# Optimization experiments

Measured on AMD Instinct MI355X. Metric: run time of the kernel, lower is better.

The kernel has to match this reference:

```python
import jax, jax.numpy as jnp
import numpy as np
from itertools import combinations

A = 4          # anchor_points
K = 16         # neighbor_num
INTRA = A * (A - 1) // 2   # 6
CH = INTRA * 2 + A * A     # 28 = generator channels
B, N, S = 1, 8192, 4096
CIN, COUT = 64, 128


def cdist(x):
    # pairwise euclidean distances [B,N,N], zero-safe sqrt (zero grad at d=0)
    sq = jnp.sum(x * x, -1)
    d2 = sq[:, :, None] + sq[:, None, :] - 2.0 * jnp.einsum('bnc,bmc->bnm', x, x)
    d2 = jnp.maximum(d2, 0.0)
    m = d2 > 0
    return jnp.where(m, jnp.sqrt(jnp.where(m, d2, 1.0)), 0.0)


def index_points(points, idx):
    # points [B,N,...], idx [B,*] -> [B,*,...]
    return jax.vmap(lambda p, i: p[i])(points, idx)


def index_points_dists(dists, i1, i2):
    # dists [B,N,N]; result[b,...] = dists[b, i1[b,...], i2[b,...]]
    i1, i2 = jnp.broadcast_arrays(i1, i2)
    return jax.vmap(lambda d, a, b: d[a, b])(dists, i1, i2)


def generator(xyz):
    # RotationInvariantDistFea.forward(xyz, concat_raw_relative_fea=True)
    D = cdist(xyz)
    neg_nd, ni = jax.lax.top_k(-D, K)   # K >= A; smallest-K, sorted ascending
    nd = -neg_nd
    ai = ni[:, :, :A]
    # intra-anchor dists: dists to anchors 1..A-1 plus pairwise dists among them
    subs = [index_points_dists(D, ai[:, :, pi], ai[:, :, pj])[:, :, None]
            for pi, pj in combinations(range(1, A), 2)]
    intra = jnp.concatenate([nd[:, :, 1:A]] + subs, axis=2)  # [B,P,6]
    # inter-anchor dists: center anchors x neighbor anchors -> [B,P,K,A*A]
    nai = index_points(ai, ni)                                # [B,P,K,A]
    inter = index_points_dists(D, ai[:, :, None, :, None],
                               nai[:, :, :, None, :]).reshape(D.shape[0], D.shape[1], K, A * A)
    center = jnp.broadcast_to(intra[:, :, None, :], (intra.shape[0], intra.shape[1], K, INTRA))
    rf = jnp.concatenate([center, index_points(intra, ni), inter], axis=3)  # [B,P,K,28]
    return rf, ni, D


def mlp(x, W, b, g, be, act):
    # Linear + BatchNorm1d (training mode: stats over batch*points) + optional leaky_relu(0.2)
    y = x @ W + b
    mu = jnp.mean(y, (0, 1))
    var = jnp.var(y, (0, 1))
    y = (y - mu) * jax.lax.rsqrt(var + 1e-5) * g + be
    return jax.nn.leaky_relu(y, 0.2) if act else y


def forward(xyz, feature, sample_indexes, Ww, bw, gw, betaw, Wb, bb, gb, betab, Wo, bo, go, betao):
    rf_before, ni_before, D_before = generator(xyz)
    intra_before = rf_before[:, :, 0, :INTRA]
    xyz_s = index_points(xyz, sample_indexes)
    feat = index_points(feature, sample_indexes)
    intra_before = index_points(intra_before, sample_indexes)
    rf_after, ni_after, _ = generator(xyz_s)
    intra_after = rf_after[:, :, 0, :INTRA]
    a_before = index_points(ni_before[:, :, :A], sample_indexes)                  # [B,S,A]
    a_after = jax.vmap(lambda s, a: s[a])(sample_indexes, ni_after[:, :, :A])     # map to global idx
    inter = index_points_dists(D_before, a_before[:, :, :, None],
                               a_after[:, :, None, :]).reshape(B, S, A * A)
    adf = jnp.concatenate([intra_before, intra_after, inter], axis=2)             # [B,S,28]
    w = mlp(adf, Ww, bw, gw, betaw, False)
    bia = mlp(adf, Wb, bb, gb, betab, False)
    feat = jax.nn.leaky_relu(feat * w + bia, 0.2)
    feat = jnp.concatenate([feat, adf], axis=2)                                   # [B,S,92]
    feat = mlp(feat, Wo, bo, go, betao, True)                                     # [B,S,128]
    return xyz_s, feat, rf_after, ni_after


def setup_inputs():
    key = jax.random.key(0)
    ks = jax.random.split(key, 8)
    xyz = jax.random.normal(ks[0], (B, N, 3), jnp.float32)
    feature = jax.random.normal(ks[1], (B, N, CIN), jnp.float32)
    sample_indexes = jnp.stack([jax.random.permutation(jax.random.fold_in(ks[2], i), N)[:S]
                                for i in range(B)]).astype(jnp.int32)

    def lin(k, cin, cout):
        k1, k2 = jax.random.split(k)
        W = jax.random.normal(k1, (cin, cout), jnp.float32) / np.float32(np.sqrt(cin))
        b = jax.random.normal(k2, (cout,), jnp.float32) * 0.01
        return W, b, jnp.ones((cout,), jnp.float32), jnp.zeros((cout,), jnp.float32)

    Ww, bw, gw, betaw = lin(ks[5], CH, CIN)
    Wb, bb, gb, betab = lin(ks[6], CH, CIN)
    Wo, bo, go, betao = lin(ks[7], CH + CIN, COUT)
    return dict(xyz=xyz, feature=feature, sample_indexes=sample_indexes,
                Ww=Ww, bw=bw, gw=gw, betaw=betaw,
                Wb=Wb, bb=bb, gb=gb, betab=betab,
                Wo=Wo, bo=bo, go=go, betao=betao)


def reference(xyz, feature, sample_indexes, Ww, bw, gw, betaw, Wb, bb, gb, betab, Wo, bo, go, betao):
    return forward(xyz, feature, sample_indexes, Ww, bw, gw, betaw, Wb, bb, gb, betab, Wo, bo, go, betao)
```

## Files before the change

### kernel.cpp

```cpp
#include <hip/hip_runtime.h>
#include <hip/hip_bf16.h>
#include <math.h>

#define N_PTS 8192
#define S_PTS 4096
typedef unsigned long long u64;
typedef unsigned u32;

__device__ __forceinline__ float d2_f32_gram(const float4 a, const float4 b) {
    float dot = __fadd_rn(__fadd_rn(__fmul_rn(a.x, b.x), __fmul_rn(a.y, b.y)),
                          __fmul_rn(a.z, b.z));
    float d2 = __fsub_rn(__fadd_rn(a.w, b.w), __fmul_rn(2.0f, dot));
    return fmaxf(d2, 0.0f);
}

__device__ __forceinline__ float pair_dist_f(const float4 a, const float4 b) {
    float d2 = d2_f32_gram(a, b);
    return d2 > 0.0f ? __fsqrt_rn(d2) : 0.0f;
}

__global__ __launch_bounds__(256) void stage_kernel(
        const float* __restrict__ xyz, const int* __restrict__ sidx,
        float4* __restrict__ cb, float4* __restrict__ ca,
        float* __restrict__ out_xyz_s) {
    int i = blockIdx.x * blockDim.x + threadIdx.x;
    if (i < N_PTS) {
        float x = xyz[i * 3 + 0], y = xyz[i * 3 + 1], z = xyz[i * 3 + 2];
        float sq = __fadd_rn(__fadd_rn(__fmul_rn(x, x), __fmul_rn(y, y)),
                             __fmul_rn(z, z));
        cb[i] = make_float4(x, y, z, sq);
    }
    if (i < S_PTS) {
        int si = sidx[i];
        float x = xyz[si * 3 + 0], y = xyz[si * 3 + 1], z = xyz[si * 3 + 2];
        float sq = __fadd_rn(__fadd_rn(__fmul_rn(x, x), __fmul_rn(y, y)),
                             __fmul_rn(z, z));
        ca[i] = make_float4(x, y, z, sq);
        out_xyz_s[i * 3 + 0] = x;
        out_xyz_s[i * 3 + 1] = y;
        out_xyz_s[i * 3 + 2] = z;
    }
}


template <int KOUT, int ITERS>
__device__ u64 knn_full_ladder(const float4 q, const float4* __restrict__ cand,
                               int lane) {
    u32 Lk[KOUT], Li[KOUT];
#pragma unroll
    for (int j = 0; j < KOUT; ++j) { Lk[j] = 0xFFFFFFFFu; Li[j] = 0xFFFFFFFFu; }
    int c = lane;
    for (int tt = 0; tt < ITERS; ++tt, c += 64) {
        float d2 = d2_f32_gram(q, cand[c]);
        float Df = d2 > 0.0f ? __fsqrt_rn(d2) : 0.0f;
        u32 kb = __float_as_uint(Df);
        if (kb < Lk[KOUT - 1]) {
#pragma unroll
            for (int j = KOUT - 1; j >= 1; --j) {
                bool up = kb < Lk[j - 1], ins = kb < Lk[j];
                Lk[j] = up ? Lk[j - 1] : (ins ? kb : Lk[j]);
                Li[j] = up ? Li[j - 1] : (ins ? (u32)c : Li[j]);
            }
            bool i0 = kb < Lk[0];
            Lk[0] = i0 ? kb : Lk[0];
            Li[0] = i0 ? (u32)c : Li[0];
        }
    }
    u64 Lu[KOUT];
#pragma unroll
    for (int j = 0; j < KOUT; ++j) Lu[j] = ((u64)Lk[j] << 32) | (u64)Li[j];
    u64 res = ~0ull;
#pragma unroll
    for (int r = 0; r < KOUT; ++r) {
        u64 m = Lu[0];
#pragma unroll
        for (int off = 32; off >= 1; off >>= 1) {
            u64 o = __shfl_xor(m, off, 64);
            m = (o < m) ? o : m;
        }
        if (lane == r) res = m;
        if (Lu[0] == m) {
#pragma unroll
            for (int j = 0; j < KOUT - 1; ++j) Lu[j] = Lu[j + 1];
            Lu[KOUT - 1] = ~0ull;
        }
    }
    return res;
}

template <int K, int NC>
__device__ u64 final_select(const float4 qq, const float4* __restrict__ cand,
                            const u64* bufq, u32 cnt, int lane) {
    if (cnt <= 64u) {
        u64 v = (lane < (int)cnt) ? bufq[lane] : ~0ull;
#pragma unroll
        for (int k = 2; k <= 64; k <<= 1) {
#pragma unroll
            for (int j2 = k >> 1; j2 >= 1; j2 >>= 1) {
                u64 o = __shfl_xor(v, j2, 64);
                bool keepMin = (((lane & j2) == 0) == ((lane & k) == 0));
                bool less = o < v;
                v = keepMin ? (less ? o : v) : (less ? v : o);
            }
        }
        return v;
    } else if (cnt <= 256u) {
        u64 L0 = ~0ull, L1 = ~0ull, L2 = ~0ull, L3 = ~0ull;
        for (u32 mm = lane; mm < cnt; mm += 64) {
            u64 kk = bufq[mm];
            if (kk < L3) {
                if (kk < L1) {
                    L3 = L2; L2 = L1;
                    if (kk < L0) { L1 = L0; L0 = kk; } else L1 = kk;
                } else {
                    if (kk < L2) { L3 = L2; L2 = kk; } else L3 = kk;
                }
            }
        }
        u64 res = ~0ull;
#pragma unroll
        for (int r = 0; r < K; ++r) {
            u64 mr = L0;
#pragma unroll
            for (int off = 32; off >= 1; off >>= 1) {
                u64 o = __shfl_xor(mr, off, 64);
                mr = (o < mr) ? o : mr;
            }
            if (lane == r) res = mr;
            if (L0 == mr) { L0 = L1; L1 = L2; L2 = L3; L3 = ~0ull; }
        }
        return res;
    }
    return knn_full_ladder<K, NC / 64>(qq, cand, lane);
}

template <int J, int K, int NC, int Q>
__device__ __forceinline__ u64 knn_selectq(
        const float4* qs, const float4* __restrict__ cand, int t,
        u32* mins, u64* buf, u32* shm) {
    int lane = t & 63, wid = t >> 6;
    u32 d2b[Q][J];
    u32 m[Q];
#pragma unroll
    for (int qi = 0; qi < Q; ++qi) m[qi] = 0xFFFFFFFFu;
#pragma unroll
    for (int j = 0; j < J; ++j) {
        float4 c = cand[t + 256 * j];
#pragma unroll
        for (int qi = 0; qi < Q; ++qi) {
            u32 b = __float_as_uint(d2_f32_gram(qs[qi], c));
            d2b[qi][j] = b;
            m[qi] = b < m[qi] ? b : m[qi];
        }
    }
#pragma unroll
    for (int qi = 0; qi < Q; ++qi) mins[qi * 256 + t] = m[qi];
    __syncthreads();
    if (wid < Q) {
        const u32* mq = mins + wid * 256;
        u32 v = mq[lane];
        u32 v2 = mq[lane + 64];  v = v2 < v ? v2 : v;
        v2 = mq[lane + 128];     v = v2 < v ? v2 : v;
        v2 = mq[lane + 192];     v = v2 < v ? v2 : v;
#pragma unroll
        for (int k = 2; k <= 64; k <<= 1) {
#pragma unroll
            for (int j2 = k >> 1; j2 >= 1; j2 >>= 1) {
                u32 o = __shfl_xor(v, j2, 64);
                bool keepMin = (((lane & j2) == 0) == ((lane & k) == 0));
                bool less = o < v;
                v = keepMin ? (less ? o : v) : (less ? v : o);
            }
        }
        if (lane == K - 1) shm[wid] = v;
    }
    __syncthreads();
    u32 tau[Q], c[Q], x[Q];
#pragma unroll
    for (int qi = 0; qi < Q; ++qi) {
        tau[qi] = shm[qi];
        u32 cc = 0;
#pragma unroll
        for (int j = 0; j < J; ++j) cc += (d2b[qi][j] <= tau[qi]) ? 1u : 0u;
        c[qi] = cc;
        u32 xx = cc;
#pragma unroll
        for (int off = 1; off < 64; off <<= 1) {
            u32 y = __shfl_up(xx, off, 64);
            if (lane >= off) xx += y;
        }
        x[qi] = xx;
        if (lane == 63) shm[Q + qi * 4 + wid] = xx;
    }
    __syncthreads();
    u32 cnt[Q];
#pragma unroll
    for (int qi = 0; qi < Q; ++qi) {
        u32 base = x[qi] - c[qi];
        for (int w = 0; w < wid; ++w) base += shm[Q + qi * 4 + w];
        cnt[qi] = shm[Q + qi * 4 + 0] + shm[Q + qi * 4 + 1] +
                  shm[Q + qi * 4 + 2] + shm[Q + qi * 4 + 3];
        if (cnt[qi] <= 256u) {
            u32 off = base;
#pragma unroll
            for (int j = 0; j < J; ++j) {
                if (d2b[qi][j] <= tau[qi]) {
                    float d2 = __uint_as_float(d2b[qi][j]);
                    float D = d2 > 0.0f ? __fsqrt_rn(d2) : 0.0f;
                    buf[qi * 256 + off++] = ((u64)__float_as_uint(D) << 32) |
                                            (u64)(u32)(t + 256 * j);
                }
            }
        }
    }
    __syncthreads();
    u64 res = ~0ull;
#pragma unroll
    for (int qi = 0; qi < Q; ++qi)
        if (wid == qi)
            res = final_select<K, NC>(qs[qi], cand, buf + qi * 256, cnt[qi], lane);
    return res;
}

__global__ __launch_bounds__(256, 4) void knn_kernel(
        const float4* __restrict__ cb, const float4* __restrict__ ca,
        const int* __restrict__ sidx,
        u64* __restrict__ stage_b4,
        int* __restrict__ ni_i, float* __restrict__ intra_after,
        float* __restrict__ out_ni) {
    __shared__ u32 mins[4 * 256];
    __shared__ u64 buf[4 * 256];
    __shared__ u32 shm[24];
    int t = threadIdx.x, lane = t & 63, wid = t >> 6;
    int bid = blockIdx.x;
    if (bid < S_PTS / 4) {
        int s0 = bid * 4;
        float4 qs[4];
#pragma unroll
        for (int qi = 0; qi < 4; ++qi) qs[qi] = ca[s0 + qi];
        u64 res = knn_selectq<16, 16, 4096, 4>(qs, ca, t, mins, buf, shm);
        if (wid < 4) {
            int s = s0 + wid;
            int idx = (int)(res & 0xffffffffull);
            if (lane < 16) {
                ni_i[s * 16 + lane] = idx;
                out_ni[s * 16 + lane] = (float)idx;
            }
            if (lane >= 1 && lane < 4)
                intra_after[s * 6 + (lane - 1)] =
                    __uint_as_float((u32)(res >> 32));
            int i1 = __shfl(idx, 1, 64);
            int i2 = __shfl(idx, 2, 64);
            int i3 = __shfl(idx, 3, 64);
            if (lane < 3) {
                int pa = (lane == 2) ? i2 : i1;
                int pb = (lane == 0) ? i2 : i3;
                intra_after[s * 6 + 3 + lane] = pair_dist_f(ca[pa], ca[pb]);
            }
        }
    } else {
        int idx2 = bid - S_PTS / 4;
        int qg = idx2 >> 1;
        int h = idx2 & 1;
        int s0 = qg * 4;
        float4 qs[4];
#pragma unroll
        for (int qi = 0; qi < 4; ++qi) qs[qi] = cb[sidx[s0 + qi]];
        u64 res = knn_selectq<16, 4, 4096, 4>(qs, cb + h * 4096, t, mins, buf, shm);
        if (wid < 4 && lane < 4) {
            int s = s0 + wid;
            stage_b4[s * 8 + h * 4 + lane] = res + (u64)(h * 4096);
        }
    }
}

__device__ __forceinline__ void cswap_u64(u64& x, u64& y) {
    u64 lo = x < y ? x : y;
    u64 hi = x < y ? y : x;
    x = lo; y = hi;
}

__global__ __launch_bounds__(256) void merge_before_kernel(
        const u64* __restrict__ stage_b4, const float4* __restrict__ cb,
        int* __restrict__ a_before, float* __restrict__ intra_before) {
    int s = blockIdx.x * 256 + threadIdx.x;
    const u64* p = stage_b4 + s * 8;
    u64 a0 = p[0], a1 = p[1], a2 = p[2], a3 = p[3];
    u64 b0 = p[4], b1 = p[5], b2 = p[6], b3 = p[7];
    u64 c0 = a0 < b3 ? a0 : b3;
    u64 c1 = a1 < b2 ? a1 : b2;
    u64 c2 = a2 < b1 ? a2 : b1;
    u64 c3 = a3 < b0 ? a3 : b0;
    cswap_u64(c0, c1); cswap_u64(c2, c3);
    cswap_u64(c0, c2); cswap_u64(c1, c3);
    cswap_u64(c1, c2);
    int i0 = (int)(c0 & 0xffffffffull);
    int i1 = (int)(c1 & 0xffffffffull);
    int i2 = (int)(c2 & 0xffffffffull);
    int i3 = (int)(c3 & 0xffffffffull);
    a_before[s * 4 + 0] = i0;
    a_before[s * 4 + 1] = i1;
    a_before[s * 4 + 2] = i2;
    a_before[s * 4 + 3] = i3;
    intra_before[s * 6 + 0] = __uint_as_float((u32)(c1 >> 32));
    intra_before[s * 6 + 1] = __uint_as_float((u32)(c2 >> 32));
    intra_before[s * 6 + 2] = __uint_as_float((u32)(c3 >> 32));
    float4 p1 = cb[i1], p2 = cb[i2], p3 = cb[i3];
    intra_before[s * 6 + 3] = pair_dist_f(p1, p2);
    intra_before[s * 6 + 4] = pair_dist_f(p1, p3);
    intra_before[s * 6 + 5] = pair_dist_f(p2, p3);
}

__global__ __launch_bounds__(256) void assemble_kernel(
        const float4* __restrict__ ca, const float4* __restrict__ cb,
        const int* __restrict__ ni_i, const float* __restrict__ intra_after,
        const int* __restrict__ a_before, const float* __restrict__ intra_before,
        const int* __restrict__ sidx,
        float* __restrict__ out_rf, float* __restrict__ adf) {
    __shared__ int s_ni[4][16];
    __shared__ float s_rf[4][16 * 28];
    __shared__ float s_ia[4][8];
    int t = threadIdx.x, wid = t >> 6, lane = t & 63;
    int s = blockIdx.x * 4 + wid;
    if (lane < 16) s_ni[wid][lane] = ni_i[s * 16 + lane];
    if (lane < 6) s_ia[wid][lane] = intra_after[s * 6 + lane];
    __syncthreads();

    int k = lane >> 2, qq = lane & 3;
    int nai_q = ni_i[s_ni[wid][k] * 16 + qq];
    float4 pq = ca[nai_q];
#pragma unroll
    for (int p = 0; p < 4; ++p) {
        float4 pp = ca[s_ni[wid][p]];
        s_rf[wid][k * 28 + 12 + p * 4 + qq] = pair_dist_f(pp, pq);
    }
    for (int idx = lane; idx < 16 * 12; idx += 64) {
        int kk = idx / 12, c = idx % 12;
        float v = (c < 6) ? s_ia[wid][c] : intra_after[s_ni[wid][kk] * 6 + (c - 6)];
        s_rf[wid][kk * 28 + c] = v;
    }
    if (lane < 16) {
        int p = lane >> 2, q2 = lane & 3;
        int ib = a_before[s * 4 + p];
        int ia = sidx[s_ni[wid][q2]];
        adf[s * 28 + 12 + lane] = pair_dist_f(cb[ib], cb[ia]);
    } else if (lane >= 32 && lane < 38) {
        adf[s * 28 + (lane - 32)] = intra_before[s * 6 + (lane - 32)];
    } else if (lane >= 40 && lane < 46) {
        adf[s * 28 + 6 + (lane - 40)] = s_ia[wid][lane - 40];
    }
    __syncthreads();
    const int base = s * 16 * 28;
    for (int idx = lane; idx < 16 * 28; idx += 64) out_rf[base + idx] = s_rf[wid][idx];
}

__global__ __launch_bounds__(256) void mlp1_kernel(
        const float* __restrict__ adf,
        const float* __restrict__ Ww, const float* __restrict__ bw,
        const float* __restrict__ Wb, const float* __restrict__ bb,
        float* __restrict__ y_wb,
        float* __restrict__ part1, float* __restrict__ part2) {
    __shared__ float sW[28 * 128];
    __shared__ float sb[128];
    __shared__ float sA[32 * 28];
    __shared__ float red[32][128];
    int t = threadIdx.x;
    for (int i = t; i < 28 * 128; i += 256) {
        int k = i >> 7, c = i & 127;
        sW[i] = (c < 64) ? Ww[k * 64 + c] : Wb[k * 64 + (c - 64)];
    }
    if (t < 128) sb[t] = (t < 64) ? bw[t] : bb[t - 64];
    int s0 = blockIdx.x * 32;
    for (int i = t; i < 32 * 28; i += 256) sA[i] = adf[s0 * 28 + i];
    __syncthreads();
    int sl = t >> 3, grp = t & 7;
    int s = s0 + sl;
    float acc[16];
#pragma unroll
    for (int k = 0; k < 16; ++k) acc[k] = sb[grp * 16 + k];
    for (int k2 = 0; k2 < 28; ++k2) {
        float a = sA[sl * 28 + k2];
#pragma unroll
        for (int k = 0; k < 16; ++k)
            acc[k] = fmaf(a, sW[k2 * 128 + grp * 16 + k], acc[k]);
    }
#pragma unroll
    for (int k = 0; k < 16; ++k) {
        y_wb[(grp * 16 + k) * 4096 + s] = acc[k];
        red[sl][grp * 16 + k] = acc[k];
    }
    __syncthreads();
    if (t < 128) {
        float s1 = 0.0f, s2 = 0.0f;
#pragma unroll 8
        for (int r = 0; r < 32; ++r) {
            float v = red[r][t];
            s1 += v;
            s2 = fmaf(v, v, s2);
        }
        part1[blockIdx.x * 128 + t] = s1;
        part2[blockIdx.x * 128 + t] = s2;
    }
}

__global__ __launch_bounds__(256) void mlp2_kernel(
        const float* __restrict__ y_wb,
        const float* __restrict__ part1, const float* __restrict__ part2,
        const float* __restrict__ gw, const float* __restrict__ betaw,
        const float* __restrict__ gb, const float* __restrict__ betab,
        const float* __restrict__ feature, const int* __restrict__ sidx,
        const float* __restrict__ adf,
        const float* __restrict__ Wo, const float* __restrict__ bo,
        float* __restrict__ y_o) {
    __shared__ float sW[92 * 128];
    __shared__ float t2[16 * 129];
    __shared__ float scat[16 * 92];
    __shared__ float s_sc[128], s_sh[128];
    int t = threadIdx.x;
    int s0 = blockIdx.x * 16;
    if (t < 128) {
        float s1 = 0.0f, s2 = 0.0f;
        for (int b = 0; b < 128; ++b) {
            s1 += part1[b * 128 + t];
            s2 += part2[b * 128 + t];
        }
        float mean = s1 * (1.0f / 4096.0f);
        float var = s2 * (1.0f / 4096.0f) - mean * mean;
        float g = (t < 64) ? gw[t] : gb[t - 64];
        float be = (t < 64) ? betaw[t] : betab[t - 64];
        float sc = g / sqrtf(var + 1e-5f);
        s_sc[t] = sc;
        s_sh[t] = be - mean * sc;
    }
    for (int i = t; i < 92 * 128; i += 256) sW[i] = Wo[i];
    __syncthreads();
    for (int i = t; i < 16 * 128; i += 256) {
        int row = i & 15, c = i >> 4;
        t2[row * 129 + c] = fmaf(y_wb[c * 4096 + s0 + row], s_sc[c], s_sh[c]);
    }
    __syncthreads();
    for (int rr = 0; rr < 16; rr += 4) {
        int r = rr + (t >> 6);
        int c = t & 63;
        int si = sidx[s0 + r];
        float f = feature[si * 64 + c];
        float v = fmaf(f, t2[r * 129 + c], t2[r * 129 + 64 + c]);
        scat[r * 92 + c] = v >= 0.0f ? v : 0.2f * v;
    }
    for (int i = t; i < 16 * 28; i += 256) {
        int row = i / 28, k = i % 28;
        scat[row * 92 + 64 + k] = adf[(s0 + row) * 28 + k];
    }
    __syncthreads();
    int r = t >> 4, cg = t & 15;
    float acc[8];
#pragma unroll
    for (int j = 0; j < 8; ++j) acc[j] = bo[cg * 8 + j];
    for (int c = 0; c < 92; ++c) {
        float a = scat[r * 92 + c];
#pragma unroll
        for (int j = 0; j < 8; ++j)
            acc[j] = fmaf(a, sW[c * 128 + cg * 8 + j], acc[j]);
    }
    int s = s0 + r;
#pragma unroll
    for (int j = 0; j < 8; ++j) y_o[(cg * 8 + j) * 4096 + s] = acc[j];
}

__global__ __launch_bounds__(256) void stats_final_kernel(
        const float* __restrict__ y_o,
        const float* __restrict__ go, const float* __restrict__ betao,
        float* __restrict__ out_feat) {
    int c = blockIdx.x;
    const float* p = y_o + c * 4096;
    float s1 = 0.0f, s2 = 0.0f;
    for (int i = threadIdx.x; i < 4096; i += 256) {
        float v = p[i];
        s1 += v;
        s2 = fmaf(v, v, s2);
    }
    __shared__ float l1[256], l2[256];
    __shared__ float s_sc, s_sh;
    l1[threadIdx.x] = s1;
    l2[threadIdx.x] = s2;
    __syncthreads();
    for (int off = 128; off; off >>= 1) {
        if (threadIdx.x < off) {
            l1[threadIdx.x] += l1[threadIdx.x + off];
            l2[threadIdx.x] += l2[threadIdx.x + off];
        }
        __syncthreads();
    }
    if (threadIdx.x == 0) {
        float mean = l1[0] * (1.0f / 4096.0f);
        float var = l2[0] * (1.0f / 4096.0f) - mean * mean;
        float sc = go[c] / sqrtf(var + 1e-5f);
        s_sc = sc;
        s_sh = betao[c] - mean * sc;
    }
    __syncthreads();
    float sc = s_sc, sh = s_sh;
    for (int i = threadIdx.x; i < 4096; i += 256) {
        float v = fmaf(p[i], sc, sh);
        v = v >= 0.0f ? v : 0.2f * v;
        out_feat[i * 128 + c] = v;
    }
}

extern "C" void kernel_launch(void* const* d_in, const int* in_sizes, int n_in,
                              void* d_out, int out_size, void* d_ws, size_t ws_size,
                              hipStream_t stream) {
    const float* xyz = (const float*)d_in[0];
    const float* feature = (const float*)d_in[1];
    const int* sidx = (const int*)d_in[2];
    const float* Ww = (const float*)d_in[3];
    const float* bw = (const float*)d_in[4];
    const float* gw = (const float*)d_in[5];
    const float* betaw = (const float*)d_in[6];
    const float* Wb = (const float*)d_in[7];
    const float* bb = (const float*)d_in[8];
    const float* gb = (const float*)d_in[9];
    const float* betab = (const float*)d_in[10];
    const float* Wo = (const float*)d_in[11];
    const float* bo = (const float*)d_in[12];
    const float* go = (const float*)d_in[13];
    const float* betao = (const float*)d_in[14];

    float* out = (float*)d_out;
    float* out_xyz = out;
    float* out_feat = out + 12288;
    float* out_rf = out + 12288 + 524288;
    float* out_ni = out + 12288 + 524288 + 1835008;

    float* ws = (float*)d_ws;
    float4* cb = (float4*)ws;
    float4* ca = (float4*)(ws + 32768);
    int* a_before = (int*)(ws + 49152);
    float* intra_before = ws + 65536;
    int* ni_i = (int*)(ws + 90112);
    float* intra_after = ws + 155648;
    float* adf = ws + 180224;
    float* y_wb = ws + 294912;
    float* y_o = ws + 819200;
    float* part1 = ws + 1343488;
    float* part2 = ws + 1359872;
    u64* stage_b4 = (u64*)(ws + 1376256);

    stage_kernel<<<32, 256, 0, stream>>>(xyz, sidx, cb, ca, out_xyz);
    knn_kernel<<<S_PTS / 4 + 2048, 256, 0, stream>>>(
        cb, ca, sidx, stage_b4, ni_i, intra_after, out_ni);
    merge_before_kernel<<<16, 256, 0, stream>>>(stage_b4, cb, a_before,
                                                intra_before);
    assemble_kernel<<<1024, 256, 0, stream>>>(ca, cb, ni_i, intra_after, a_before,
                                              intra_before, sidx, out_rf, adf);
    mlp1_kernel<<<128, 256, 0, stream>>>(adf, Ww, bw, Wb, bb, y_wb, part1, part2);
    mlp2_kernel<<<256, 256, 0, stream>>>(y_wb, part1, part2, gw, betaw, gb, betab,
                                         feature, sidx, adf, Wo, bo, y_o);
    stats_final_kernel<<<128, 256, 0, stream>>>(y_o, go, betao, out_feat);
}
```

Measured before the change: 166.9 us.

## Reuse sampled-set distances for 8192-point kNN and search only unsampled complement

The 4-NN search over all 8192 points previously scanned both halves of the cloud in separate blocks. Now the sampled points' distances, already computed for the 16-NN over the sample set, also yield a top-4 (mapped through sidx). Only the 4096 unsampled points, compacted via a bitmask and prefix scan into a separate array with a permutation map, get their own scan. This cuts the candidate-distance work and the grid from 3072 to 2048 blocks. The cost is two extra small kernels, more shared memory per block, and an extra index indirection in the selection paths.

```diff
diff --git a/kernel.cpp b/kernel.cpp
--- a/kernel.cpp
+++ b/kernel.cpp
@@ -21,9 +21,10 @@
 
 __global__ __launch_bounds__(256) void stage_kernel(
         const float* __restrict__ xyz, const int* __restrict__ sidx,
-        float4* __restrict__ cb, float4* __restrict__ ca,
+        float4* __restrict__ cb, float4* __restrict__ ca, u64* __restrict__ mkG,
         float* __restrict__ out_xyz_s) {
     int i = blockIdx.x * blockDim.x + threadIdx.x;
+    if (i < 128) mkG[i] = 0ull;
     if (i < N_PTS) {
         float x = xyz[i * 3 + 0], y = xyz[i * 3 + 1], z = xyz[i * 3 + 2];
         float sq = __fadd_rn(__fadd_rn(__fmul_rn(x, x), __fmul_rn(y, y)),
@@ -42,33 +43,69 @@
     }
 }
 
+__global__ __launch_bounds__(256) void mask_kernel(
+        const int* __restrict__ sidx, u64* __restrict__ mkG) {
+    int i = blockIdx.x * 256 + threadIdx.x;
+    int si = sidx[i];
+    atomicOr(&mkG[si >> 6], 1ull << (si & 63));
+}
+
+__global__ __launch_bounds__(256) void build_kernel(
+        const u64* __restrict__ mkG, const float4* __restrict__ cb,
+        float4* __restrict__ cbu, int* __restrict__ permu) {
+    __shared__ u64 w[128];
+    __shared__ u32 pre[128];
+    __shared__ u32 wtot0;
+    int t = threadIdx.x, lane = t & 63;
+    if (t < 128) w[t] = mkG[t];
+    __syncthreads();
+    if (t < 128) {
+        u32 cnt = 64u - (u32)__popcll(w[t]);
+        u32 x = cnt;
+#pragma unroll
+        for (int off = 1; off < 64; off <<= 1) {
+            u32 y = __shfl_up(x, off, 64);
+            if (lane >= off) x += y;
+        }
+        pre[t] = x - cnt;
+        if (t == 63) wtot0 = x;
+    }
+    __syncthreads();
+    if (t >= 64 && t < 128) pre[t] += wtot0;
+    __syncthreads();
+    int c = blockIdx.x * 256 + t;
+    u64 word = w[c >> 6];
+    if (!((word >> (c & 63)) & 1ull)) {
+        u64 below = word & ((1ull << (c & 63)) - 1ull);
+        u32 inword = (u32)(c & 63) - (u32)__popcll(below);
+        u32 pos = pre[c >> 6] + inword;
+        cbu[pos] = cb[c];
+        permu[pos] = c;
+    }
+}
+
 
 template <int KOUT, int ITERS>
-__device__ u64 knn_full_ladder(const float4 q, const float4* __restrict__ cand,
-                               int lane) {
-    u32 Lk[KOUT], Li[KOUT];
-#pragma unroll
-    for (int j = 0; j < KOUT; ++j) { Lk[j] = 0xFFFFFFFFu; Li[j] = 0xFFFFFFFFu; }
+__device__ u64 knn_full_ladder_key(const float4 q, const float4* __restrict__ cand,
+                                   const int* __restrict__ idxmap, int lane) {
+    u64 Lu[KOUT];
+#pragma unroll
+    for (int j = 0; j < KOUT; ++j) Lu[j] = ~0ull;
     int c = lane;
     for (int tt = 0; tt < ITERS; ++tt, c += 64) {
         float d2 = d2_f32_gram(q, cand[c]);
         float Df = d2 > 0.0f ? __fsqrt_rn(d2) : 0.0f;
-        u32 kb = __float_as_uint(Df);
-        if (kb < Lk[KOUT - 1]) {
+        u32 idx = idxmap ? (u32)idxmap[c] : (u32)c;
+        u64 kk = ((u64)__float_as_uint(Df) << 32) | (u64)idx;
+        if (kk < Lu[KOUT - 1]) {
 #pragma unroll
             for (int j = KOUT - 1; j >= 1; --j) {
-                bool up = kb < Lk[j - 1], ins = kb < Lk[j];
-                Lk[j] = up ? Lk[j - 1] : (ins ? kb : Lk[j]);
-                Li[j] = up ? Li[j - 1] : (ins ? (u32)c : Li[j]);
-            }
-            bool i0 = kb < Lk[0];
-            Lk[0] = i0 ? kb : Lk[0];
-            Li[0] = i0 ? (u32)c : Li[0];
-        }
-    }
-    u64 Lu[KOUT];
-#pragma unroll
-    for (int j = 0; j < KOUT; ++j) Lu[j] = ((u64)Lk[j] << 32) | (u64)Li[j];
+                bool up = kk < Lu[j - 1], ins = kk < Lu[j];
+                Lu[j] = up ? Lu[j - 1] : (ins ? kk : Lu[j]);
+            }
+            if (kk < Lu[0]) Lu[0] = kk;
+        }
+    }
     u64 res = ~0ull;
 #pragma unroll
     for (int r = 0; r < KOUT; ++r) {
@@ -90,6 +127,7 @@
 
 template <int K, int NC>
 __device__ u64 final_select(const float4 qq, const float4* __restrict__ cand,
+                            const int* __restrict__ idxmap,
                             const u64* bufq, u32 cnt, int lane) {
     if (cnt <= 64u) {
         u64 v = (lane < (int)cnt) ? bufq[lane] : ~0ull;
@@ -131,12 +169,31 @@
         }
         return res;
     }
-    return knn_full_ladder<K, NC / 64>(qq, cand, lane);
+    return knn_full_ladder_key<K, NC / 64>(qq, cand, idxmap, lane);
+}
+
+__device__ __forceinline__ u32 sort64_colmin(const u32* mq, int lane) {
+    u32 v = mq[lane];
+    u32 v2 = mq[lane + 64];  v = v2 < v ? v2 : v;
+    v2 = mq[lane + 128];     v = v2 < v ? v2 : v;
+    v2 = mq[lane + 192];     v = v2 < v ? v2 : v;
+#pragma unroll
+    for (int k = 2; k <= 64; k <<= 1) {
+#pragma unroll
+        for (int j2 = k >> 1; j2 >= 1; j2 >>= 1) {
+            u32 o = __shfl_xor(v, j2, 64);
+            bool keepMin = (((lane & j2) == 0) == ((lane & k) == 0));
+            bool less = o < v;
+            v = keepMin ? (less ? o : v) : (less ? v : o);
+        }
+    }
+    return v;
 }
 
 template <int J, int K, int NC, int Q>
 __device__ __forceinline__ u64 knn_selectq(
-        const float4* qs, const float4* __restrict__ cand, int t,
+        const float4* qs, const float4* __restrict__ cand,
+        const int* __restrict__ idxmap, int t,
         u32* mins, u64* buf, u32* shm) {
     int lane = t & 63, wid = t >> 6;
     u32 d2b[Q][J];
@@ -157,21 +214,7 @@
     for (int qi = 0; qi < Q; ++qi) mins[qi * 256 + t] = m[qi];
     __syncthreads();
     if (wid < Q) {
-        const u32* mq = mins + wid * 256;
-        u32 v = mq[lane];
-        u32 v2 = mq[lane + 64];  v = v2 < v ? v2 : v;
-        v2 = mq[lane + 128];     v = v2 < v ? v2 : v;
-        v2 = mq[lane + 192];     v = v2 < v ? v2 : v;
-#pragma unroll
-        for (int k = 2; k <= 64; k <<= 1) {
-#pragma unroll
-            for (int j2 = k >> 1; j2 >= 1; j2 >>= 1) {
-                u32 o = __shfl_xor(v, j2, 64);
-                bool keepMin = (((lane & j2) == 0) == ((lane & k) == 0));
-                bool less = o < v;
-                v = keepMin ? (less ? o : v) : (less ? v : o);
-            }
-        }
+        u32 v = sort64_colmin(mins + wid * 256, lane);
         if (lane == K - 1) shm[wid] = v;
     }
     __syncthreads();
@@ -207,8 +250,10 @@
                 if (d2b[qi][j] <= tau[qi]) {
                     float d2 = __uint_as_float(d2b[qi][j]);
                     float D = d2 > 0.0f ? __fsqrt_rn(d2) : 0.0f;
-                    buf[qi * 256 + off++] = ((u64)__float_as_uint(D) << 32) |
-                                            (u64)(u32)(t + 256 * j);
+                    int cc2 = t + 256 * j;
+                    u32 idx = idxmap ? (u32)idxmap[cc2] : (u32)cc2;
+                    buf[qi * 256 + off++] =
+                        ((u64)__float_as_uint(D) << 32) | (u64)idx;
                 }
             }
         }
@@ -218,19 +263,127 @@
 #pragma unroll
     for (int qi = 0; qi < Q; ++qi)
         if (wid == qi)
-            res = final_select<K, NC>(qs[qi], cand, buf + qi * 256, cnt[qi], lane);
+            res = final_select<K, NC>(qs[qi], cand, idxmap, buf + qi * 256,
+                                      cnt[qi], lane);
     return res;
 }
 
+template <int Q>
+__device__ __forceinline__ void knn_select_dual(
+        const float4* qs, const float4* __restrict__ ca,
+        const int* __restrict__ sidx, int t,
+        u32* mins, u64* bufA, u64* bufB, u32* shm,
+        u64& resA, u64& resB) {
+    const int J = 16;
+    int lane = t & 63, wid = t >> 6;
+    u32 d2b[Q][J];
+    u32 m[Q];
+#pragma unroll
+    for (int qi = 0; qi < Q; ++qi) m[qi] = 0xFFFFFFFFu;
+#pragma unroll
+    for (int j = 0; j < J; ++j) {
+        float4 c4 = ca[t + 256 * j];
+#pragma unroll
+        for (int qi = 0; qi < Q; ++qi) {
+            u32 b = __float_as_uint(d2_f32_gram(qs[qi], c4));
+            d2b[qi][j] = b;
+            m[qi] = b < m[qi] ? b : m[qi];
+        }
+    }
+#pragma unroll
+    for (int qi = 0; qi < Q; ++qi) mins[qi * 256 + t] = m[qi];
+    __syncthreads();
+    if (wid < Q) {
+        u32 v = sort64_colmin(mins + wid * 256, lane);
+        if (lane == 15) shm[wid] = v;
+        if (lane == 3) shm[Q + wid] = v;
+    }
+    __syncthreads();
+    u32 tA[Q], tB[Q], cA[Q], cB[Q], xA[Q], xB[Q];
+#pragma unroll
+    for (int qi = 0; qi < Q; ++qi) {
+        tA[qi] = shm[qi];
+        tB[qi] = shm[Q + qi];
+        u32 ca_ = 0, cb_ = 0;
+#pragma unroll
+        for (int j = 0; j < J; ++j) {
+            ca_ += (d2b[qi][j] <= tA[qi]) ? 1u : 0u;
+            cb_ += (d2b[qi][j] <= tB[qi]) ? 1u : 0u;
+        }
+        cA[qi] = ca_; cB[qi] = cb_;
+        u32 xa = ca_, xb = cb_;
+#pragma unroll
+        for (int off = 1; off < 64; off <<= 1) {
+            u32 ya = __shfl_up(xa, off, 64);
+            u32 yb = __shfl_up(xb, off, 64);
+            if (lane >= off) { xa += ya; xb += yb; }
+        }
+        xA[qi] = xa; xB[qi] = xb;
+        if (lane == 63) {
+            shm[2 * Q + qi * 4 + wid] = xa;
+            shm[2 * Q + 4 * Q + qi * 4 + wid] = xb;
+        }
+    }
+    __syncthreads();
+    u32 cntA[Q], cntB[Q];
+#pragma unroll
+    for (int qi = 0; qi < Q; ++qi) {
+        u32 bA = xA[qi] - cA[qi], bB = xB[qi] - cB[qi];
+        for (int w = 0; w < wid; ++w) {
+            bA += shm[2 * Q + qi * 4 + w];
+            bB += shm[2 * Q + 4 * Q + qi * 4 + w];
+        }
+        cntA[qi] = shm[2 * Q + qi * 4 + 0] + shm[2 * Q + qi * 4 + 1] +
+                   shm[2 * Q + qi * 4 + 2] + shm[2 * Q + qi * 4 + 3];
+        cntB[qi] = shm[2 * Q + 4 * Q + qi * 4 + 0] + shm[2 * Q + 4 * Q + qi * 4 + 1] +
+                   shm[2 * Q + 4 * Q + qi * 4 + 2] + shm[2 * Q + 4 * Q + qi * 4 + 3];
+        if (cntA[qi] <= 256u) {
+            u32 off = bA;
+#pragma unroll
+            for (int j = 0; j < J; ++j) {
+                if (d2b[qi][j] <= tA[qi]) {
+                    float d2 = __uint_as_float(d2b[qi][j]);
+                    float D = d2 > 0.0f ? __fsqrt_rn(d2) : 0.0f;
+                    bufA[qi * 256 + off++] = ((u64)__float_as_uint(D) << 32) |
+                                             (u64)(u32)(t + 256 * j);
+                }
+            }
+        }
+        if (cntB[qi] <= 256u) {
+            u32 off = bB;
+#pragma unroll
+            for (int j = 0; j < J; ++j) {
+                if (d2b[qi][j] <= tB[qi]) {
+                    float d2 = __uint_as_float(d2b[qi][j]);
+                    float D = d2 > 0.0f ? __fsqrt_rn(d2) : 0.0f;
+                    bufB[qi * 256 + off++] = ((u64)__float_as_uint(D) << 32) |
+                                             (u64)(u32)sidx[t + 256 * j];
+                }
+            }
+        }
+    }
+    __syncthreads();
+    resA = ~0ull; resB = ~0ull;
+#pragma unroll
+    for (int qi = 0; qi < Q; ++qi)
+        if (wid == qi) {
+            resA = final_select<16, 4096>(qs[qi], ca, (const int*)nullptr,
+                                          bufA + qi * 256, cntA[qi], lane);
+            resB = final_select<4, 4096>(qs[qi], ca, sidx,
+                                         bufB + qi * 256, cntB[qi], lane);
+        }
+}
+
 __global__ __launch_bounds__(256, 4) void knn_kernel(
-        const float4* __restrict__ cb, const float4* __restrict__ ca,
-        const int* __restrict__ sidx,
+        const float4* __restrict__ ca, const float4* __restrict__ cbu,
+        const int* __restrict__ sidx, const int* __restrict__ permu,
         u64* __restrict__ stage_b4,
         int* __restrict__ ni_i, float* __restrict__ intra_after,
         float* __restrict__ out_ni) {
     __shared__ u32 mins[4 * 256];
-    __shared__ u64 buf[4 * 256];
-    __shared__ u32 shm[24];
+    __shared__ u64 bufA[4 * 256];
+    __shared__ u64 bufB[4 * 256];
+    __shared__ u32 shm[48];
     int t = threadIdx.x, lane = t & 63, wid = t >> 6;
     int bid = blockIdx.x;
     if (bid < S_PTS / 4) {
@@ -238,17 +391,18 @@
         float4 qs[4];
 #pragma unroll
         for (int qi = 0; qi < 4; ++qi) qs[qi] = ca[s0 + qi];
-        u64 res = knn_selectq<16, 16, 4096, 4>(qs, ca, t, mins, buf, shm);
+        u64 resA, resB;
+        knn_select_dual<4>(qs, ca, sidx, t, mins, bufA, bufB, shm, resA, resB);
         if (wid < 4) {
             int s = s0 + wid;
-            int idx = (int)(res & 0xffffffffull);
+            int idx = (int)(resA & 0xffffffffull);
             if (lane < 16) {
                 ni_i[s * 16 + lane] = idx;
                 out_ni[s * 16 + lane] = (float)idx;
             }
             if (lane >= 1 && lane < 4)
                 intra_after[s * 6 + (lane - 1)] =
-                    __uint_as_float((u32)(res >> 32));
+                    __uint_as_float((u32)(resA >> 32));
             int i1 = __shfl(idx, 1, 64);
             int i2 = __shfl(idx, 2, 64);
             int i3 = __shfl(idx, 3, 64);
@@ -257,20 +411,16 @@
                 int pb = (lane == 0) ? i2 : i3;
                 intra_after[s * 6 + 3 + lane] = pair_dist_f(ca[pa], ca[pb]);
             }
+            if (lane < 4) stage_b4[s * 8 + lane] = resB;
         }
     } else {
-        int idx2 = bid - S_PTS / 4;
-        int qg = idx2 >> 1;
-        int h = idx2 & 1;
-        int s0 = qg * 4;
+        int s0 = (bid - S_PTS / 4) * 4;
         float4 qs[4];
 #pragma unroll
-        for (int qi = 0; qi < 4; ++qi) qs[qi] = cb[sidx[s0 + qi]];
-        u64 res = knn_selectq<16, 4, 4096, 4>(qs, cb + h * 4096, t, mins, buf, shm);
-        if (wid < 4 && lane < 4) {
-            int s = s0 + wid;
-            stage_b4[s * 8 + h * 4 + lane] = res + (u64)(h * 4096);
-        }
+        for (int qi = 0; qi < 4; ++qi) qs[qi] = ca[s0 + qi];
+        u64 res = knn_selectq<16, 4, 4096, 4>(qs, cbu, permu, t, mins, bufA, shm);
+        if (wid < 4 && lane < 4)
+            stage_b4[(s0 + wid) * 8 + 4 + lane] = res;
     }
 }
 
@@ -545,10 +695,15 @@
     float* part1 = ws + 1343488;
     float* part2 = ws + 1359872;
     u64* stage_b4 = (u64*)(ws + 1376256);
-
-    stage_kernel<<<32, 256, 0, stream>>>(xyz, sidx, cb, ca, out_xyz);
-    knn_kernel<<<S_PTS / 4 + 2048, 256, 0, stream>>>(
-        cb, ca, sidx, stage_b4, ni_i, intra_after, out_ni);
+    float4* cbu = (float4*)(ws + 1441792);
+    int* permu = (int*)(ws + 1458176);
+    u64* mkG = (u64*)(ws + 1462272);
+
+    stage_kernel<<<32, 256, 0, stream>>>(xyz, sidx, cb, ca, mkG, out_xyz);
+    mask_kernel<<<16, 256, 0, stream>>>(sidx, mkG);
+    build_kernel<<<32, 256, 0, stream>>>(mkG, cb, cbu, permu);
+    knn_kernel<<<2048, 256, 0, stream>>>(ca, cbu, sidx, permu, stage_b4,
+                                         ni_i, intra_after, out_ni);
     merge_before_kernel<<<16, 256, 0, stream>>>(stage_b4, cb, a_before,
                                                 intra_before);
     assemble_kernel<<<1024, 256, 0, stream>>>(ca, cb, ni_i, intra_after, a_before,
```

Result: no change. 169.2 us (+1.4%).
